# Kernel tuning notes

Measured on AMD Instinct MI355X. Metric: run time of the kernel, lower is better.

## Reference

```python
import jax, jax.numpy as jnp
import numpy as np

N = 100000
E = 1600000
DIN = 128
DH = 128
DOUT = 32
G = 64
EPS = 1e-5


def setup_inputs() -> dict:
    key = jax.random.key(0)
    ks = jax.random.split(key, 12)
    x = jax.random.normal(ks[0], (N, DIN), dtype=jnp.float32)
    edge_index = jax.random.randint(ks[1], (2, E), 0, N, dtype=jnp.int64)
    batch = jnp.sort(jax.random.randint(ks[2], (N,), 0, G, dtype=jnp.int64))
    # GCNConv weights (glorot-ish) + zero bias
    W1 = jax.random.normal(ks[3], (DIN, DH), dtype=jnp.float32) * (2.0 / (DIN + DH)) ** 0.5
    b1 = jnp.zeros((DH,), jnp.float32)
    W2 = jax.random.normal(ks[4], (DH, DH), dtype=jnp.float32) * (2.0 / (DH + DH)) ** 0.5
    b2 = jnp.zeros((DH,), jnp.float32)
    # BatchNorm affine params
    g1 = jnp.ones((DH,), jnp.float32); be1 = jnp.zeros((DH,), jnp.float32)
    g2 = jnp.ones((DH,), jnp.float32); be2 = jnp.zeros((DH,), jnp.float32)
    # Linear heads: kaiming normal fan_in relu, bias=0.001
    fw1 = jax.random.normal(ks[5], (DH, DH), dtype=jnp.float32) * (2.0 / DH) ** 0.5
    fb1 = jnp.full((DH,), 0.001, jnp.float32)
    fw2 = jax.random.normal(ks[6], (DH, DOUT), dtype=jnp.float32) * (2.0 / DH) ** 0.5
    fb2 = jnp.full((DOUT,), 0.001, jnp.float32)
    return dict(x=x, edge_index=edge_index, batch=batch, W1=W1, b1=b1, W2=W2, b2=b2,
                g1=g1, be1=be1, g2=g2, be2=be2, fw1=fw1, fb1=fb1, fw2=fw2, fb2=fb2)


def _gcn(x, src, dst, dinv, W, b):
    h = x @ W  # [N, F]
    norm = dinv[src] * dinv[dst]  # [E+N]
    agg = jax.ops.segment_sum(h[src] * norm[:, None], dst, num_segments=N)
    return agg + b


def _bn(h, gamma, beta):
    mu = h.mean(axis=0)
    var = h.var(axis=0)  # biased, matches torch BN training mode
    return (h - mu) * jax.lax.rsqrt(var + EPS) * gamma + beta


def reference(x, edge_index, batch, W1, b1, W2, b2, g1, be1, g2, be2, fw1, fb1, fw2, fb2):
    # add self-loops (PyG GCNConv default)
    loops = jnp.arange(N, dtype=edge_index.dtype)
    src = jnp.concatenate([edge_index[0], loops])
    dst = jnp.concatenate([edge_index[1], loops])
    deg = jax.ops.segment_sum(jnp.ones_like(dst, dtype=x.dtype), dst, num_segments=N)
    dinv = jnp.where(deg > 0, jax.lax.rsqrt(deg), 0.0)

    h = jax.nn.relu(_bn(_gcn(x, src, dst, dinv, W1, b1), g1, be1))
    h = jax.nn.relu(_bn(_gcn(h, src, dst, dinv, W2, b2), g2, be2))

    # global mean pool over graph ids
    sums = jax.ops.segment_sum(h, batch, num_segments=G)
    cnt = jax.ops.segment_sum(jnp.ones((N,), h.dtype), batch, num_segments=G)
    pooled = sums / jnp.maximum(cnt, 1.0)[:, None]  # [G, DH]

    z = jax.nn.relu(pooled @ fw1 + fb1)
    return jax.nn.softmax(z @ fw2 + fb2, axis=1)
```

## Files before the change

### kernel.cpp

```cpp
#include <hip/hip_runtime.h>
#include <hip/hip_bf16.h>
#include <stdint.h>

#define NN 100000
#define NE 1600000
#define DH 128
#define DOUT 32
#define NG 64
#define EPS 1e-5f

#define SCAN_BLK 1024
#define SCAN_NB ((NN + SCAN_BLK - 1) / SCAN_BLK)
#define NBUCKET 32
#define NRANGE 4
#define RANGE_SZ (NN / NRANGE)

typedef __attribute__((ext_vector_type(8))) unsigned short ushort8;
typedef __attribute__((ext_vector_type(8))) short bfv8;
typedef __attribute__((ext_vector_type(4))) float f32x4;
typedef __attribute__((ext_vector_type(4))) int intv4;
typedef __attribute__((ext_vector_type(2))) unsigned int uintv2;

__device__ __forceinline__ float b2f(unsigned short u) {
    return __uint_as_float(((unsigned int)u) << 16);
}
__device__ __forceinline__ unsigned int f2b(float f) {
    unsigned int u = __float_as_uint(f);
    return (u + 0x7fffu + ((u >> 16) & 1u)) >> 16;
}
__device__ __forceinline__ float blo(unsigned int v) { return __uint_as_float(v << 16); }
__device__ __forceinline__ float bhi(unsigned int v) { return __uint_as_float(v & 0xffff0000u); }


__global__ void k_count(const int* __restrict__ ei_dst, int* __restrict__ cnt) {
    int range = blockIdx.x & (NRANGE - 1);
    int lo = range * RANGE_SZ, hi = lo + RANGE_SZ;
    int i = (blockIdx.x >> 2) * blockDim.x + threadIdx.x;
    int stride = (gridDim.x >> 2) * blockDim.x;
    const intv4* d4 = reinterpret_cast<const intv4*>(ei_dst);
    for (int e = i; e < NE / 4; e += stride) {
        intv4 d = __builtin_nontemporal_load(d4 + e);
        if (d.x >= lo && d.x < hi) atomicAdd(&cnt[d.x], 1);
        if (d.y >= lo && d.y < hi) atomicAdd(&cnt[d.y], 1);
        if (d.z >= lo && d.z < hi) atomicAdd(&cnt[d.z], 1);
        if (d.w >= lo && d.w < hi) atomicAdd(&cnt[d.w], 1);
    }
}

__global__ void k_fill(const int* __restrict__ ei, int* __restrict__ cursor, int* __restrict__ csr) {
    int range = blockIdx.x & (NRANGE - 1);
    int lo = range * RANGE_SZ, hi = lo + RANGE_SZ;
    int i = (blockIdx.x >> 2) * blockDim.x + threadIdx.x;
    int stride = (gridDim.x >> 2) * blockDim.x;
    const intv4* s4 = reinterpret_cast<const intv4*>(ei);
    const intv4* d4 = reinterpret_cast<const intv4*>(ei + NE);
    for (int e = i; e < NE / 4; e += stride) {
        intv4 s = __builtin_nontemporal_load(s4 + e);
        intv4 d = __builtin_nontemporal_load(d4 + e);
        if (d.x >= lo && d.x < hi) csr[atomicAdd(&cursor[d.x], 1)] = s.x;
        if (d.y >= lo && d.y < hi) csr[atomicAdd(&cursor[d.y], 1)] = s.y;
        if (d.z >= lo && d.z < hi) csr[atomicAdd(&cursor[d.z], 1)] = s.z;
        if (d.w >= lo && d.w < hi) csr[atomicAdd(&cursor[d.w], 1)] = s.w;
    }
}

__global__ void k_gbound(const int* __restrict__ batch, int* __restrict__ first, int* __restrict__ last) {
    int i = blockIdx.x * blockDim.x + threadIdx.x;
    if (i >= NN) return;
    int g = batch[i];
    if (i == 0 || batch[i - 1] != g) first[g] = i;
    if (i == NN - 1 || batch[i + 1] != g) last[g] = i + 1;
}

__global__ void k_scan_partial(const int* __restrict__ cnt, int* __restrict__ bsum) {
    __shared__ int sdata[256];
    int blk = blockIdx.x, t = threadIdx.x;
    int base = blk * SCAN_BLK + t * 4;
    int s = 0;
#pragma unroll
    for (int q = 0; q < 4; q++) { int idx = base + q; if (idx < NN) s += cnt[idx]; }
    sdata[t] = s; __syncthreads();
    for (int o = 128; o; o >>= 1) { if (t < o) sdata[t] += sdata[t + o]; __syncthreads(); }
    if (t == 0) bsum[blk] = sdata[0];
}

__global__ void k_scan_top(const int* __restrict__ bsum, int* __restrict__ bscan, int* __restrict__ rowptr,
                           const int* __restrict__ first, const int* __restrict__ last, int* __restrict__ gcnt) {
    __shared__ int sd[128];
    int t = threadIdx.x;
    int v = (t < SCAN_NB) ? bsum[t] : 0;
    sd[t] = v; __syncthreads();
    for (int o = 1; o < 128; o <<= 1) {
        int add = (t >= o) ? sd[t - o] : 0;
        __syncthreads();
        sd[t] += add;
        __syncthreads();
    }
    if (t < SCAN_NB) bscan[t] = sd[t] - v;
    if (t == 127) rowptr[NN] = sd[127];
    if (t < NG) gcnt[t] = last[t] - first[t];
}

__global__ void k_scan_final(int* __restrict__ cnt, const int* __restrict__ bscan,
                             int* __restrict__ rowptr, float* __restrict__ dinv) {
    __shared__ int sdata[256];
    int blk = blockIdx.x, t = threadIdx.x;
    int base = blk * SCAN_BLK + t * 4;
    int v[4]; int s = 0;
#pragma unroll
    for (int q = 0; q < 4; q++) { int idx = base + q; v[q] = (idx < NN) ? cnt[idx] : 0; s += v[q]; }
    sdata[t] = s; __syncthreads();
    for (int o = 1; o < 256; o <<= 1) {
        int add = (t >= o) ? sdata[t - o] : 0;
        __syncthreads();
        sdata[t] += add;
        __syncthreads();
    }
    int offset = bscan[blk] + sdata[t] - s;
#pragma unroll
    for (int q = 0; q < 4; q++) {
        int idx = base + q;
        if (idx < NN) {
            rowptr[idx] = offset;
            cnt[idx] = offset;
            dinv[idx] = rsqrtf((float)(v[q] + 1));
            offset += v[q];
        }
    }
}


__global__ void k_prepw(const float* __restrict__ W1, const float* __restrict__ W2,
                        unsigned short* __restrict__ WT1, unsigned short* __restrict__ WT2) {
    int i = blockIdx.x * blockDim.x + threadIdx.x;
    int sel = i >> 14;
    int j = i & 16383;
    int k = j >> 7, n = j & 127;
    const float* W = sel ? W2 : W1;
    unsigned short* WT = sel ? WT2 : WT1;
    WT[n * 128 + k] = (unsigned short)f2b(W[j]);
}


template <bool BN, typename AT>
__global__ __launch_bounds__(256) void k_gemm(const AT* __restrict__ A, const unsigned short* __restrict__ WTg,
                                              unsigned short* __restrict__ C, const float* __restrict__ rowscale,
                                              const float* __restrict__ scale, const float* __restrict__ shift) {
    __shared__ unsigned char lds[65536];
    unsigned char* As = lds;
    unsigned char* Ws = lds + 32768;
    int row0 = blockIdx.x * 128;
    int t = threadIdx.x;
    int l = t & 63;
    int w = t >> 6;

    if constexpr (sizeof(AT) == 4) {
#pragma unroll
        for (int q = 0; q < 16; q++) {
            int idx = q * 256 + t;
            int r = idx >> 5, c4 = idx & 31;
            float4 v = make_float4(0.f, 0.f, 0.f, 0.f);
            if (row0 + r < NN) v = reinterpret_cast<const float4*>(A)[(size_t)(row0 + r) * 32 + c4];
            ushort4 u;
            u.x = (unsigned short)f2b(v.x);
            u.y = (unsigned short)f2b(v.y);
            u.z = (unsigned short)f2b(v.z);
            u.w = (unsigned short)f2b(v.w);
            int off = r * 256 + ((c4 * 8) ^ ((r & 7) << 4));
            *reinterpret_cast<ushort4*>(As + off) = u;
        }
    } else {
#pragma unroll
        for (int q = 0; q < 8; q++) {
            int idx = q * 256 + t;
            int r = idx >> 4, c8 = idx & 15;
// ... 38 lines not shown
            a[m] = *reinterpret_cast<const bfv8*>(As + r * 256 + (kb ^ ((r & 7) << 4)));
        }
        bfv8 b[8];
#pragma unroll
        for (int n = 0; n < 8; n++) {
            int r = n * 16 + lrow;
            b[n] = *reinterpret_cast<const bfv8*>(Ws + r * 256 + (kb ^ ((r & 7) << 4)));
        }
#pragma unroll
        for (int m = 0; m < 2; m++)
#pragma unroll
            for (int n = 0; n < 8; n++)
                acc[m][n] = __builtin_amdgcn_mfma_f32_16x16x32_bf16(a[m], b[n], acc[m][n], 0, 0, 0);
    }

#pragma unroll
    for (int m = 0; m < 2; m++) {
#pragma unroll
        for (int rr = 0; rr < 4; rr++) {
            int grow = row0 + w * 32 + m * 16 + (l >> 4) * 4 + rr;
            if (grow < NN) {
                float rs = rowscale[grow];
#pragma unroll
                for (int n = 0; n < 8; n++) {
                    int col = n * 16 + (l & 15);
                    C[(size_t)grow * DH + col] = (unsigned short)f2b(acc[m][n][rr] * rs);
                }
            }
        }
    }
}


__global__ __launch_bounds__(256) void k_aggregate(const unsigned short* __restrict__ h, const int* __restrict__ rowptr,
                                                   const int* __restrict__ csr, const float* __restrict__ dinv,
                                                   unsigned short* __restrict__ agg, float* __restrict__ stats) {
    int lane = threadIdx.x & 63;
    int wv = threadIdx.x >> 6;
    int half = lane >> 5;
    int sl = lane & 31;
    const uintv2* h64 = reinterpret_cast<const uintv2*>(h);
    uintv2* agg64 = reinterpret_cast<uintv2*>(agg);
    int wid = blockIdx.x * 4 + wv;
    int nw = gridDim.x * 4;
    long long tlo = ((long long)wid * NE) / nw;
    long long thi = (wid == nw - 1) ? (long long)NE + 1 : (((long long)(wid + 1) * NE) / nw);

    int lo = 0, hi = NN;
    while (lo < hi) {
        int mid = (lo + hi) >> 1;
        if (rowptr[mid] < (int)tlo) lo = mid + 1; else hi = mid;
    }

    float s0 = 0.f, s1 = 0.f, s2 = 0.f, s3 = 0.f;
    float q0 = 0.f, q1 = 0.f, q2 = 0.f, q3 = 0.f;
    for (int i = lo; i < NN; i++) {
        int row = rowptr[i];
        if (row >= (int)thi) break;
        int end = rowptr[i + 1];
        int len = end - row;
        float di = dinv[i];
        float a0 = 0.f, a1 = 0.f, a2 = 0.f, a3 = 0.f;
        if (half == 0) {
            uintv2 sv = h64[(size_t)i * 32 + sl];
            a0 = blo(sv.x); a1 = bhi(sv.x); a2 = blo(sv.y); a3 = bhi(sv.y);
        }
        int hc = (len + 1 - half) >> 1;
        int tt = 0;
        for (; tt + 8 <= hc; tt += 8) {
            int eA = row + (tt << 1) + half;
            int n0 = __builtin_nontemporal_load(&csr[eA]);
            int n1 = __builtin_nontemporal_load(&csr[eA + 2]);
            int n2 = __builtin_nontemporal_load(&csr[eA + 4]);
            int n3 = __builtin_nontemporal_load(&csr[eA + 6]);
            int n4 = __builtin_nontemporal_load(&csr[eA + 8]);
            int n5 = __builtin_nontemporal_load(&csr[eA + 10]);
            int n6 = __builtin_nontemporal_load(&csr[eA + 12]);
            int n7 = __builtin_nontemporal_load(&csr[eA + 14]);
            uintv2 v0 = h64[(size_t)n0 * 32 + sl];
            uintv2 v1 = h64[(size_t)n1 * 32 + sl];
            uintv2 v2 = h64[(size_t)n2 * 32 + sl];
            uintv2 v3 = h64[(size_t)n3 * 32 + sl];
            uintv2 v4 = h64[(size_t)n4 * 32 + sl];
            uintv2 v5 = h64[(size_t)n5 * 32 + sl];
            uintv2 v6 = h64[(size_t)n6 * 32 + sl];
            uintv2 v7 = h64[(size_t)n7 * 32 + sl];
            a0 += blo(v0.x); a1 += bhi(v0.x); a2 += blo(v0.y); a3 += bhi(v0.y);
            a0 += blo(v1.x); a1 += bhi(v1.x); a2 += blo(v1.y); a3 += bhi(v1.y);
            a0 += blo(v2.x); a1 += bhi(v2.x); a2 += blo(v2.y); a3 += bhi(v2.y);
            a0 += blo(v3.x); a1 += bhi(v3.x); a2 += blo(v3.y); a3 += bhi(v3.y);
            a0 += blo(v4.x); a1 += bhi(v4.x); a2 += blo(v4.y); a3 += bhi(v4.y);
            a0 += blo(v5.x); a1 += bhi(v5.x); a2 += blo(v5.y); a3 += bhi(v5.y);
            a0 += blo(v6.x); a1 += bhi(v6.x); a2 += blo(v6.y); a3 += bhi(v6.y);
            a0 += blo(v7.x); a1 += bhi(v7.x); a2 += blo(v7.y); a3 += bhi(v7.y);
        }
        for (; tt + 4 <= hc; tt += 4) {
            int eA = row + (tt << 1) + half;
            int n0 = __builtin_nontemporal_load(&csr[eA]);
            int n1 = __builtin_nontemporal_load(&csr[eA + 2]);
            int n2 = __builtin_nontemporal_load(&csr[eA + 4]);
            int n3 = __builtin_nontemporal_load(&csr[eA + 6]);
            uintv2 v0 = h64[(size_t)n0 * 32 + sl];
            uintv2 v1 = h64[(size_t)n1 * 32 + sl];
            uintv2 v2 = h64[(size_t)n2 * 32 + sl];
            uintv2 v3 = h64[(size_t)n3 * 32 + sl];
            a0 += blo(v0.x); a1 += bhi(v0.x); a2 += blo(v0.y); a3 += bhi(v0.y);
            a0 += blo(v1.x); a1 += bhi(v1.x); a2 += blo(v1.y); a3 += bhi(v1.y);
            a0 += blo(v2.x); a1 += bhi(v2.x); a2 += blo(v2.y); a3 += bhi(v2.y);
            a0 += blo(v3.x); a1 += bhi(v3.x); a2 += blo(v3.y); a3 += bhi(v3.y);
        }
        for (; tt < hc; tt++) {
            int e = row + (tt << 1) + half;
            int n = __builtin_nontemporal_load(&csr[e]);
            uintv2 v = h64[(size_t)n * 32 + sl];
            a0 += blo(v.x); a1 += bhi(v.x); a2 += blo(v.y); a3 += bhi(v.y);
        }
        a0 += __shfl_xor(a0, 32);
        a1 += __shfl_xor(a1, 32);
        a2 += __shfl_xor(a2, 32);
        a3 += __shfl_xor(a3, 32);
        a0 *= di; a1 *= di; a2 *= di; a3 *= di;
        if (half == 0) {
            uintv2 o;
            o.x = f2b(a0) | (f2b(a1) << 16);
            o.y = f2b(a2) | (f2b(a3) << 16);
            __builtin_nontemporal_store(o, agg64 + ((size_t)i * 32 + sl));
            s0 += a0; q0 += a0 * a0;
            s1 += a1; q1 += a1 * a1;
            s2 += a2; q2 += a2 * a2;
            s3 += a3; q3 += a3 * a3;
        }
    }
    if (half == 0) {
        float* b = stats + (size_t)(wid & (NBUCKET - 1)) * 256;
        atomicAdd(&b[sl * 4 + 0], s0);
        atomicAdd(&b[sl * 4 + 1], s1);
        atomicAdd(&b[sl * 4 + 2], s2);
        atomicAdd(&b[sl * 4 + 3], s3);
        atomicAdd(&b[128 + sl * 4 + 0], q0);
        atomicAdd(&b[128 + sl * 4 + 1], q1);
        atomicAdd(&b[128 + sl * 4 + 2], q2);
        atomicAdd(&b[128 + sl * 4 + 3], q3);
    }
}

__global__ void k_bnparams(const float* __restrict__ stats, const float* __restrict__ gamma,
                           const float* __restrict__ beta, float* __restrict__ scale, float* __restrict__ shift) {
    int j = threadIdx.x;
    float su = 0.f, sq = 0.f;
    for (int b = 0; b < NBUCKET; b++) { su += stats[b * 256 + j]; sq += stats[b * 256 + 128 + j]; }
    float mu = su * (1.f / NN);
    float var = sq * (1.f / NN) - mu * mu;
    float rs = rsqrtf(var + EPS);
    float sc = rs * gamma[j];
    scale[j] = sc;
    shift[j] = beta[j] - mu * sc;
}


#define POOL_CHUNK 64

__global__ __launch_bounds__(64) void k_pool(const unsigned short* __restrict__ agg, const int* __restrict__ batch,
                                             const float* __restrict__ scale, const float* __restrict__ shift,
                                             float* __restrict__ pooled) {
    int j = threadIdx.x;
    const unsigned int* a32 = reinterpret_cast<const unsigned int*>(agg);
    int n0 = blockIdx.x * POOL_CHUNK;
    int n1 = n0 + POOL_CHUNK; if (n1 > NN) n1 = NN;
    float sc0 = scale[j * 2], sh0 = shift[j * 2];
    float sc1 = scale[j * 2 + 1], sh1 = shift[j * 2 + 1];
    int gcur = batch[n0];
    float acc0 = 0.f, acc1 = 0.f;
    for (int i = n0; i < n1; i++) {
        int g = batch[i];
        if (g != gcur) {
            atomicAdd(&pooled[(size_t)gcur * DH + j * 2], acc0);
            atomicAdd(&pooled[(size_t)gcur * DH + j * 2 + 1], acc1);
            acc0 = acc1 = 0.f; gcur = g;
        }
        unsigned int v = a32[(size_t)i * 64 + j];
        acc0 += fmaxf(blo(v) * sc0 + sh0, 0.f);
        acc1 += fmaxf(bhi(v) * sc1 + sh1, 0.f);
    }
    atomicAdd(&pooled[(size_t)gcur * DH + j * 2], acc0);
    atomicAdd(&pooled[(size_t)gcur * DH + j * 2 + 1], acc1);
}


__global__ __launch_bounds__(128) void k_head(const float* __restrict__ pooled, const int* __restrict__ gcnt,
// ... 36 lines not shown
    const int*   batch = (const int*)d_in[2];
    const float* W1    = (const float*)d_in[3];
    const float* W2    = (const float*)d_in[5];
    const float* g1    = (const float*)d_in[7];
    const float* be1   = (const float*)d_in[8];
    const float* g2    = (const float*)d_in[9];
    const float* be2   = (const float*)d_in[10];
    const float* fw1   = (const float*)d_in[11];
    const float* fb1   = (const float*)d_in[12];
    const float* fw2   = (const float*)d_in[13];
    const float* fb2   = (const float*)d_in[14];
    float* out = (float*)d_out;

    char* w = (char*)d_ws;
    unsigned short* hbuf = (unsigned short*)w;  w += (size_t)NN * DH * 2;
    unsigned short* abuf = (unsigned short*)w;  w += (size_t)NN * DH * 2;
    int*   csr    = (int*)w;    w += (size_t)NE * 4;
    int*   rowptr = (int*)w;    w += (size_t)(NN + 1) * 4;  w = align256p(w);
    float* dinv   = (float*)w;  w += (size_t)NN * 4;
    int*   bsum   = (int*)w;    w += 512 * 4;
    int*   bscan  = (int*)w;    w += 512 * 4;
    float* scale1 = (float*)w;  w += DH * 4;
    float* shift1 = (float*)w;  w += DH * 4;
    float* scale2 = (float*)w;  w += DH * 4;
    float* shift2 = (float*)w;  w += DH * 4;
    unsigned short* WT1g = (unsigned short*)w;  w += (size_t)DH * DH * 2;
    unsigned short* WT2g = (unsigned short*)w;  w += (size_t)DH * DH * 2;
    w = align256p(w);
    char* zstart  = w;
    int*   cnt    = (int*)w;    w += (size_t)NN * 4;
    int*   gfirst = (int*)w;    w += 64 * 4;
    int*   glast  = (int*)w;    w += 64 * 4;
    int*   gcnt   = (int*)w;    w += 64 * 4;
    float* stats1 = (float*)w;  w += (size_t)NBUCKET * 256 * 4;
    float* stats2 = (float*)w;  w += (size_t)NBUCKET * 256 * 4;
    float* pooled = (float*)w;  w += (size_t)NG * DH * 4;
    size_t zbytes = (size_t)(w - zstart);
    size_t need = (size_t)(w - (char*)d_ws);
    if (ws_size < need) return;

    hipMemsetAsync(zstart, 0, zbytes, stream);

    k_prepw<<<128, 256, 0, stream>>>(W1, W2, WT1g, WT2g);
    k_count<<<1024, 256, 0, stream>>>(ei + NE, cnt);
    k_gbound<<<(NN + 255) / 256, 256, 0, stream>>>(batch, gfirst, glast);
    k_scan_partial<<<SCAN_NB, 256, 0, stream>>>(cnt, bsum);
    k_scan_top<<<1, 128, 0, stream>>>(bsum, bscan, rowptr, gfirst, glast, gcnt);
    k_scan_final<<<SCAN_NB, 256, 0, stream>>>(cnt, bscan, rowptr, dinv);
    k_fill<<<1024, 256, 0, stream>>>(ei, cnt, csr);

    int gemm_grid = (NN + 127) / 128;

    k_gemm<false, float><<<gemm_grid, 256, 0, stream>>>(x, WT1g, hbuf, dinv, nullptr, nullptr);
    k_aggregate<<<2048, 256, 0, stream>>>(hbuf, rowptr, csr, dinv, abuf, stats1);
    k_bnparams<<<1, 128, 0, stream>>>(stats1, g1, be1, scale1, shift1);

    k_gemm<true, unsigned short><<<gemm_grid, 256, 0, stream>>>(abuf, WT2g, hbuf, dinv, scale1, shift1);
    k_aggregate<<<2048, 256, 0, stream>>>(hbuf, rowptr, csr, dinv, abuf, stats2);
    k_bnparams<<<1, 128, 0, stream>>>(stats2, g2, be2, scale2, shift2);

    int pool_grid = (NN + POOL_CHUNK - 1) / POOL_CHUNK;
    k_pool<<<pool_grid, 64, 0, stream>>>(abuf, batch, scale2, shift2, pooled);
    k_head<<<NG, 128, 0, stream>>>(pooled, gcnt, fw1, fb1, fw2, fb2, out);
}
```

Before: 503.6 us.

## Fuse prep kernels, fold BN params into aggregate, process two rows per wave

Merges the degree count, graph-boundary and weight-transpose kernels into one launch, and computes the BN scale/shift in the last-finishing block of the aggregate kernel using a completion counter, which removes separate tiny launches. The aggregate loop now handles two destination rows at once with predicated 4-wide gathers, replacing the 8/4/1 unrolled tail loops. It also drops the nontemporal csr loads and agg stores and switches to 128-thread blocks. Predication wastes gather slots when the two rows differ in degree, and the last-block pattern relies on threadfence ordering.

```diff
diff --git a/kernel.cpp b/kernel.cpp
--- a/kernel.cpp
+++ b/kernel.cpp
@@ -15,6 +15,10 @@
 #define NRANGE 4
 #define RANGE_SZ (NN / NRANGE)
 
+#define PREP_COUNT_BLKS 1024
+#define PREP_GB_BLKS ((NN + 255) / 256)
+#define PREP_PW_BLKS 128
+
 typedef __attribute__((ext_vector_type(8))) unsigned short ushort8;
 typedef __attribute__((ext_vector_type(8))) short bfv8;
 typedef __attribute__((ext_vector_type(4))) float f32x4;
@@ -32,18 +36,98 @@
 __device__ __forceinline__ float bhi(unsigned int v) { return __uint_as_float(v & 0xffff0000u); }
 
 
-__global__ void k_count(const int* __restrict__ ei_dst, int* __restrict__ cnt) {
-    int range = blockIdx.x & (NRANGE - 1);
-    int lo = range * RANGE_SZ, hi = lo + RANGE_SZ;
-    int i = (blockIdx.x >> 2) * blockDim.x + threadIdx.x;
-    int stride = (gridDim.x >> 2) * blockDim.x;
-    const intv4* d4 = reinterpret_cast<const intv4*>(ei_dst);
-    for (int e = i; e < NE / 4; e += stride) {
-        intv4 d = __builtin_nontemporal_load(d4 + e);
-        if (d.x >= lo && d.x < hi) atomicAdd(&cnt[d.x], 1);
-        if (d.y >= lo && d.y < hi) atomicAdd(&cnt[d.y], 1);
-        if (d.z >= lo && d.z < hi) atomicAdd(&cnt[d.z], 1);
-        if (d.w >= lo && d.w < hi) atomicAdd(&cnt[d.w], 1);
+__global__ void k_prep(const int* __restrict__ ei_dst, int* __restrict__ cnt,
+                       const int* __restrict__ batch, int* __restrict__ gfirst, int* __restrict__ glast,
+                       const float* __restrict__ W1, const float* __restrict__ W2,
+                       unsigned short* __restrict__ WT1, unsigned short* __restrict__ WT2) {
+    int bid = blockIdx.x;
+    int t = threadIdx.x;
+    if (bid < PREP_COUNT_BLKS) {
+        int range = bid & (NRANGE - 1);
+        int lo = range * RANGE_SZ, hi = lo + RANGE_SZ;
+        int i = (bid >> 2) * 256 + t;
+        int stride = (PREP_COUNT_BLKS >> 2) * 256;
+        const intv4* d4 = reinterpret_cast<const intv4*>(ei_dst);
+        for (int e = i; e < NE / 4; e += stride) {
+            intv4 d = __builtin_nontemporal_load(d4 + e);
+            if (d.x >= lo && d.x < hi) atomicAdd(&cnt[d.x], 1);
+            if (d.y >= lo && d.y < hi) atomicAdd(&cnt[d.y], 1);
+            if (d.z >= lo && d.z < hi) atomicAdd(&cnt[d.z], 1);
+            if (d.w >= lo && d.w < hi) atomicAdd(&cnt[d.w], 1);
+        }
+    } else if (bid < PREP_COUNT_BLKS + PREP_GB_BLKS) {
+        int i = (bid - PREP_COUNT_BLKS) * 256 + t;
+        if (i < NN) {
+            int g = batch[i];
+            if (i == 0 || batch[i - 1] != g) gfirst[g] = i;
+            if (i == NN - 1 || batch[i + 1] != g) glast[g] = i + 1;
+        }
+    } else {
+        int i = (bid - PREP_COUNT_BLKS - PREP_GB_BLKS) * 256 + t;
+        int sel = i >> 14;
+        int j = i & 16383;
+        int k = j >> 7, n = j & 127;
+        const float* W = sel ? W2 : W1;
+        unsigned short* WT = sel ? WT2 : WT1;
+        WT[n * 128 + k] = (unsigned short)f2b(W[j]);
+    }
+}
+
+
+__global__ void k_scan_partial(const int* __restrict__ cnt, int* __restrict__ bsum) {
+    __shared__ int sdata[256];
+    int blk = blockIdx.x, t = threadIdx.x;
+    int base = blk * SCAN_BLK + t * 4;
+    int s = 0;
+#pragma unroll
+    for (int q = 0; q < 4; q++) { int idx = base + q; if (idx < NN) s += cnt[idx]; }
+    sdata[t] = s; __syncthreads();
+    for (int o = 128; o; o >>= 1) { if (t < o) sdata[t] += sdata[t + o]; __syncthreads(); }
+    if (t == 0) bsum[blk] = sdata[0];
+}
+
+__global__ void k_scan_top(const int* __restrict__ bsum, int* __restrict__ bscan, int* __restrict__ rowptr,
+                           const int* __restrict__ first, const int* __restrict__ last, int* __restrict__ gcnt) {
+    __shared__ int sd[128];
+    int t = threadIdx.x;
+    int v = (t < SCAN_NB) ? bsum[t] : 0;
+    sd[t] = v; __syncthreads();
+    for (int o = 1; o < 128; o <<= 1) {
+        int add = (t >= o) ? sd[t - o] : 0;
+        __syncthreads();
+        sd[t] += add;
+        __syncthreads();
+    }
+    if (t < SCAN_NB) bscan[t] = sd[t] - v;
+    if (t == 127) rowptr[NN] = sd[127];
+    if (t < NG) gcnt[t] = last[t] - first[t];
+}
+
+__global__ void k_scan_final(int* __restrict__ cnt, const int* __restrict__ bscan,
+                             int* __restrict__ rowptr, float* __restrict__ dinv) {
+    __shared__ int sdata[256];
+    int blk = blockIdx.x, t = threadIdx.x;
+    int base = blk * SCAN_BLK + t * 4;
+    int v[4]; int s = 0;
+#pragma unroll
+    for (int q = 0; q < 4; q++) { int idx = base + q; v[q] = (idx < NN) ? cnt[idx] : 0; s += v[q]; }
+    sdata[t] = s; __syncthreads();
+    for (int o = 1; o < 256; o <<= 1) {
+        int add = (t >= o) ? sdata[t - o] : 0;
+        __syncthreads();
+        sdata[t] += add;
+        __syncthreads();
+    }
+    int offset = bscan[blk] + sdata[t] - s;
+#pragma unroll
+    for (int q = 0; q < 4; q++) {
+        int idx = base + q;
+        if (idx < NN) {
+            rowptr[idx] = offset;
+            cnt[idx] = offset;
+            dinv[idx] = rsqrtf((float)(v[q] + 1));
+            offset += v[q];
+        }
     }
 }
 
@@ -64,83 +148,6 @@
     }
 }
 
-__global__ void k_gbound(const int* __restrict__ batch, int* __restrict__ first, int* __restrict__ last) {
-    int i = blockIdx.x * blockDim.x + threadIdx.x;
-    if (i >= NN) return;
-    int g = batch[i];
-    if (i == 0 || batch[i - 1] != g) first[g] = i;
-    if (i == NN - 1 || batch[i + 1] != g) last[g] = i + 1;
-}
-
-__global__ void k_scan_partial(const int* __restrict__ cnt, int* __restrict__ bsum) {
-    __shared__ int sdata[256];
-    int blk = blockIdx.x, t = threadIdx.x;
-    int base = blk * SCAN_BLK + t * 4;
-    int s = 0;
-#pragma unroll
-    for (int q = 0; q < 4; q++) { int idx = base + q; if (idx < NN) s += cnt[idx]; }
-    sdata[t] = s; __syncthreads();
-    for (int o = 128; o; o >>= 1) { if (t < o) sdata[t] += sdata[t + o]; __syncthreads(); }
-    if (t == 0) bsum[blk] = sdata[0];
-}
-
-__global__ void k_scan_top(const int* __restrict__ bsum, int* __restrict__ bscan, int* __restrict__ rowptr,
-                           const int* __restrict__ first, const int* __restrict__ last, int* __restrict__ gcnt) {
-    __shared__ int sd[128];
-    int t = threadIdx.x;
-    int v = (t < SCAN_NB) ? bsum[t] : 0;
-    sd[t] = v; __syncthreads();
-    for (int o = 1; o < 128; o <<= 1) {
-        int add = (t >= o) ? sd[t - o] : 0;
-        __syncthreads();
-        sd[t] += add;
-        __syncthreads();
-    }
-    if (t < SCAN_NB) bscan[t] = sd[t] - v;
-    if (t == 127) rowptr[NN] = sd[127];
-    if (t < NG) gcnt[t] = last[t] - first[t];
-}
-
-__global__ void k_scan_final(int* __restrict__ cnt, const int* __restrict__ bscan,
-                             int* __restrict__ rowptr, float* __restrict__ dinv) {
-    __shared__ int sdata[256];
-    int blk = blockIdx.x, t = threadIdx.x;
-    int base = blk * SCAN_BLK + t * 4;
-    int v[4]; int s = 0;
-#pragma unroll
-    for (int q = 0; q < 4; q++) { int idx = base + q; v[q] = (idx < NN) ? cnt[idx] : 0; s += v[q]; }
-    sdata[t] = s; __syncthreads();
-    for (int o = 1; o < 256; o <<= 1) {
-        int add = (t >= o) ? sdata[t - o] : 0;
-        __syncthreads();
-        sdata[t] += add;
-        __syncthreads();
-    }
-    int offset = bscan[blk] + sdata[t] - s;
-#pragma unroll
-    for (int q = 0; q < 4; q++) {
-        int idx = base + q;
-        if (idx < NN) {
-            rowptr[idx] = offset;
-            cnt[idx] = offset;
-            dinv[idx] = rsqrtf((float)(v[q] + 1));
-            offset += v[q];
-        }
-    }
-}
-
-
-__global__ void k_prepw(const float* __restrict__ W1, const float* __restrict__ W2,
-                        unsigned short* __restrict__ WT1, unsigned short* __restrict__ WT2) {
-    int i = blockIdx.x * blockDim.x + threadIdx.x;
-    int sel = i >> 14;
-    int j = i & 16383;
-    int k = j >> 7, n = j & 127;
-    const float* W = sel ? W2 : W1;
-    unsigned short* WT = sel ? WT2 : WT1;
-    WT[n * 128 + k] = (unsigned short)f2b(W[j]);
-}
-
 
 template <bool BN, typename AT>
 __global__ __launch_bounds__(256) void k_gemm(const AT* __restrict__ A, const unsigned short* __restrict__ WTg,
@@ -245,19 +252,23 @@
 }
 
 
-__global__ __launch_bounds__(256) void k_aggregate(const unsigned short* __restrict__ h, const int* __restrict__ rowptr,
+__global__ __launch_bounds__(128) void k_aggregate(const unsigned short* __restrict__ h, const int* __restrict__ rowptr,
                                                    const int* __restrict__ csr, const float* __restrict__ dinv,
-                                                   unsigned short* __restrict__ agg, float* __restrict__ stats) {
+                                                   unsigned short* __restrict__ agg, float* __restrict__ stats,
+                                                   const float* __restrict__ gamma, const float* __restrict__ beta,
+                                                   float* __restrict__ scale, float* __restrict__ shift,
+                                                   int* __restrict__ done) {
     int lane = threadIdx.x & 63;
     int wv = threadIdx.x >> 6;
     int half = lane >> 5;
     int sl = lane & 31;
     const uintv2* h64 = reinterpret_cast<const uintv2*>(h);
     uintv2* agg64 = reinterpret_cast<uintv2*>(agg);
-    int wid = blockIdx.x * 4 + wv;
-    int nw = gridDim.x * 4;
+    int wid = blockIdx.x * 2 + wv;
+    int nw = gridDim.x * 2;
     long long tlo = ((long long)wid * NE) / nw;
     long long thi = (wid == nw - 1) ? (long long)NE + 1 : (((long long)(wid + 1) * NE) / nw);
+    int thii = (int)thi;
 
     int lo = 0, hi = NN;
     while (lo < hi) {
@@ -267,82 +278,97 @@
 
     float s0 = 0.f, s1 = 0.f, s2 = 0.f, s3 = 0.f;
     float q0 = 0.f, q1 = 0.f, q2 = 0.f, q3 = 0.f;
-    for (int i = lo; i < NN; i++) {
-        int row = rowptr[i];
-        if (row >= (int)thi) break;
-        int end = rowptr[i + 1];
-        int len = end - row;
-        float di = dinv[i];
+    int i = lo;
+    int rowA = (i < NN) ? rowptr[i] : NE;
+    while (i < NN && rowA < thii) {
+        int endA = rowptr[i + 1];
+        int iB = i + 1;
+        int rowB = endA;
+        bool hasB = (iB < NN) && (rowB < thii);
+        int endB = hasB ? rowptr[iB + 1] : rowB;
+        int lenA = endA - rowA;
+        int lenB = endB - rowB;
+
+        float diA = dinv[i];
+        float diB = hasB ? dinv[iB] : 0.f;
         float a0 = 0.f, a1 = 0.f, a2 = 0.f, a3 = 0.f;
+        float b0 = 0.f, b1 = 0.f, b2 = 0.f, b3 = 0.f;
         if (half == 0) {
             uintv2 sv = h64[(size_t)i * 32 + sl];
             a0 = blo(sv.x); a1 = bhi(sv.x); a2 = blo(sv.y); a3 = bhi(sv.y);
-        }
-        int hc = (len + 1 - half) >> 1;
-        int tt = 0;
-        for (; tt + 8 <= hc; tt += 8) {
-            int eA = row + (tt << 1) + half;
-            int n0 = __builtin_nontemporal_load(&csr[eA]);
-            int n1 = __builtin_nontemporal_load(&csr[eA + 2]);
-            int n2 = __builtin_nontemporal_load(&csr[eA + 4]);
-            int n3 = __builtin_nontemporal_load(&csr[eA + 6]);
-            int n4 = __builtin_nontemporal_load(&csr[eA + 8]);
-            int n5 = __builtin_nontemporal_load(&csr[eA + 10]);
-            int n6 = __builtin_nontemporal_load(&csr[eA + 12]);
-            int n7 = __builtin_nontemporal_load(&csr[eA + 14]);
-            uintv2 v0 = h64[(size_t)n0 * 32 + sl];
-            uintv2 v1 = h64[(size_t)n1 * 32 + sl];
-            uintv2 v2 = h64[(size_t)n2 * 32 + sl];
-            uintv2 v3 = h64[(size_t)n3 * 32 + sl];
-            uintv2 v4 = h64[(size_t)n4 * 32 + sl];
-            uintv2 v5 = h64[(size_t)n5 * 32 + sl];
-            uintv2 v6 = h64[(size_t)n6 * 32 + sl];
-            uintv2 v7 = h64[(size_t)n7 * 32 + sl];
-            a0 += blo(v0.x); a1 += bhi(v0.x); a2 += blo(v0.y); a3 += bhi(v0.y);
-            a0 += blo(v1.x); a1 += bhi(v1.x); a2 += blo(v1.y); a3 += bhi(v1.y);
-            a0 += blo(v2.x); a1 += bhi(v2.x); a2 += blo(v2.y); a3 += bhi(v2.y);
-            a0 += blo(v3.x); a1 += bhi(v3.x); a2 += blo(v3.y); a3 += bhi(v3.y);
-            a0 += blo(v4.x); a1 += bhi(v4.x); a2 += blo(v4.y); a3 += bhi(v4.y);
-            a0 += blo(v5.x); a1 += bhi(v5.x); a2 += blo(v5.y); a3 += bhi(v5.y);
-            a0 += blo(v6.x); a1 += bhi(v6.x); a2 += blo(v6.y); a3 += bhi(v6.y);
-            a0 += blo(v7.x); a1 += bhi(v7.x); a2 += blo(v7.y); a3 += bhi(v7.y);
-        }
-        for (; tt + 4 <= hc; tt += 4) {
-            int eA = row + (tt << 1) + half;
-            int n0 = __builtin_nontemporal_load(&csr[eA]);
-            int n1 = __builtin_nontemporal_load(&csr[eA + 2]);
-            int n2 = __builtin_nontemporal_load(&csr[eA + 4]);
-            int n3 = __builtin_nontemporal_load(&csr[eA + 6]);
-            uintv2 v0 = h64[(size_t)n0 * 32 + sl];
-            uintv2 v1 = h64[(size_t)n1 * 32 + sl];
-            uintv2 v2 = h64[(size_t)n2 * 32 + sl];
-            uintv2 v3 = h64[(size_t)n3 * 32 + sl];
-            a0 += blo(v0.x); a1 += bhi(v0.x); a2 += blo(v0.y); a3 += bhi(v0.y);
-            a0 += blo(v1.x); a1 += bhi(v1.x); a2 += blo(v1.y); a3 += bhi(v1.y);
-            a0 += blo(v2.x); a1 += bhi(v2.x); a2 += blo(v2.y); a3 += bhi(v2.y);
-            a0 += blo(v3.x); a1 += bhi(v3.x); a2 += blo(v3.y); a3 += bhi(v3.y);
-        }
-        for (; tt < hc; tt++) {
-            int e = row + (tt << 1) + half;
-            int n = __builtin_nontemporal_load(&csr[e]);
-            uintv2 v = h64[(size_t)n * 32 + sl];
-            a0 += blo(v.x); a1 += bhi(v.x); a2 += blo(v.y); a3 += bhi(v.y);
-        }
-        a0 += __shfl_xor(a0, 32);
-        a1 += __shfl_xor(a1, 32);
-        a2 += __shfl_xor(a2, 32);
-        a3 += __shfl_xor(a3, 32);
-        a0 *= di; a1 *= di; a2 *= di; a3 *= di;
+            if (hasB) {
+                uintv2 tv = h64[(size_t)iB * 32 + sl];
+                b0 = blo(tv.x); b1 = bhi(tv.x); b2 = blo(tv.y); b3 = bhi(tv.y);
+            }
+        }
+        int hcA = (lenA + 1 - half) >> 1;
+        int hcB = hasB ? ((lenB + 1 - half) >> 1) : 0;
+        int hmU = ((lenA + 1) >> 1);
+        int hmB = ((lenB + 1) >> 1);
+        if (hasB && hmB > hmU) hmU = hmB;
+
+        for (int tt = 0; tt < hmU; tt += 4) {
+            int baseA = rowA + (tt << 1) + half;
+            int baseB = rowB + (tt << 1) + half;
+            bool pA0 = (tt + 0) < hcA, pA1 = (tt + 1) < hcA, pA2 = (tt + 2) < hcA, pA3 = (tt + 3) < hcA;
+            bool pB0 = (tt + 0) < hcB, pB1 = (tt + 1) < hcB, pB2 = (tt + 2) < hcB, pB3 = (tt + 3) < hcB;
+            int iA0 = pA0 ? csr[baseA + 0] : i;
+            int iA1 = pA1 ? csr[baseA + 2] : i;
+            int iA2 = pA2 ? csr[baseA + 4] : i;
+            int iA3 = pA3 ? csr[baseA + 6] : i;
+            int iB0 = pB0 ? csr[baseB + 0] : i;
+            int iB1 = pB1 ? csr[baseB + 2] : i;
+            int iB2 = pB2 ? csr[baseB + 4] : i;
+            int iB3 = pB3 ? csr[baseB + 6] : i;
+            uintv2 vA0 = h64[(size_t)iA0 * 32 + sl];
+            uintv2 vA1 = h64[(size_t)iA1 * 32 + sl];
+            uintv2 vA2 = h64[(size_t)iA2 * 32 + sl];
+            uintv2 vA3 = h64[(size_t)iA3 * 32 + sl];
+            uintv2 vB0 = h64[(size_t)iB0 * 32 + sl];
+            uintv2 vB1 = h64[(size_t)iB1 * 32 + sl];
+            uintv2 vB2 = h64[(size_t)iB2 * 32 + sl];
+            uintv2 vB3 = h64[(size_t)iB3 * 32 + sl];
+            a0 += pA0 ? blo(vA0.x) : 0.f; a1 += pA0 ? bhi(vA0.x) : 0.f;
+            a2 += pA0 ? blo(vA0.y) : 0.f; a3 += pA0 ? bhi(vA0.y) : 0.f;
+            a0 += pA1 ? blo(vA1.x) : 0.f; a1 += pA1 ? bhi(vA1.x) : 0.f;
+            a2 += pA1 ? blo(vA1.y) : 0.f; a3 += pA1 ? bhi(vA1.y) : 0.f;
+            a0 += pA2 ? blo(vA2.x) : 0.f; a1 += pA2 ? bhi(vA2.x) : 0.f;
+            a2 += pA2 ? blo(vA2.y) : 0.f; a3 += pA2 ? bhi(vA2.y) : 0.f;
+            a0 += pA3 ? blo(vA3.x) : 0.f; a1 += pA3 ? bhi(vA3.x) : 0.f;
+            a2 += pA3 ? blo(vA3.y) : 0.f; a3 += pA3 ? bhi(vA3.y) : 0.f;
+            b0 += pB0 ? blo(vB0.x) : 0.f; b1 += pB0 ? bhi(vB0.x) : 0.f;
+            b2 += pB0 ? blo(vB0.y) : 0.f; b3 += pB0 ? bhi(vB0.y) : 0.f;
+            b0 += pB1 ? blo(vB1.x) : 0.f; b1 += pB1 ? bhi(vB1.x) : 0.f;
+            b2 += pB1 ? blo(vB1.y) : 0.f; b3 += pB1 ? bhi(vB1.y) : 0.f;
+            b0 += pB2 ? blo(vB2.x) : 0.f; b1 += pB2 ? bhi(vB2.x) : 0.f;
+            b2 += pB2 ? blo(vB2.y) : 0.f; b3 += pB2 ? bhi(vB2.y) : 0.f;
+            b0 += pB3 ? blo(vB3.x) : 0.f; b1 += pB3 ? bhi(vB3.x) : 0.f;
+            b2 += pB3 ? blo(vB3.y) : 0.f; b3 += pB3 ? bhi(vB3.y) : 0.f;
+        }
+        a0 += __shfl_xor(a0, 32); a1 += __shfl_xor(a1, 32);
+        a2 += __shfl_xor(a2, 32); a3 += __shfl_xor(a3, 32);
+        b0 += __shfl_xor(b0, 32); b1 += __shfl_xor(b1, 32);
+        b2 += __shfl_xor(b2, 32); b3 += __shfl_xor(b3, 32);
+        a0 *= diA; a1 *= diA; a2 *= diA; a3 *= diA;
+        b0 *= diB; b1 *= diB; b2 *= diB; b3 *= diB;
         if (half == 0) {
             uintv2 o;
             o.x = f2b(a0) | (f2b(a1) << 16);
             o.y = f2b(a2) | (f2b(a3) << 16);
-            __builtin_nontemporal_store(o, agg64 + ((size_t)i * 32 + sl));
-            s0 += a0; q0 += a0 * a0;
-            s1 += a1; q1 += a1 * a1;
-            s2 += a2; q2 += a2 * a2;
-            s3 += a3; q3 += a3 * a3;
-        }
+            agg64[(size_t)i * 32 + sl] = o;
+            s0 += a0; q0 += a0 * a0; s1 += a1; q1 += a1 * a1;
+            s2 += a2; q2 += a2 * a2; s3 += a3; q3 += a3 * a3;
+            if (hasB) {
+                uintv2 p;
+                p.x = f2b(b0) | (f2b(b1) << 16);
+                p.y = f2b(b2) | (f2b(b3) << 16);
+                agg64[(size_t)iB * 32 + sl] = p;
+                s0 += b0; q0 += b0 * b0; s1 += b1; q1 += b1 * b1;
+                s2 += b2; q2 += b2 * b2; s3 += b3; q3 += b3 * b3;
+            }
+        }
+        i += hasB ? 2 : 1;
+        rowA = hasB ? endB : endA;
     }
     if (half == 0) {
         float* b = stats + (size_t)(wid & (NBUCKET - 1)) * 256;
@@ -355,19 +381,26 @@
         atomicAdd(&b[128 + sl * 4 + 2], q2);
         atomicAdd(&b[128 + sl * 4 + 3], q3);
     }
-}
-
-__global__ void k_bnparams(const float* __restrict__ stats, const float* __restrict__ gamma,
-                           const float* __restrict__ beta, float* __restrict__ scale, float* __restrict__ shift) {
-    int j = threadIdx.x;
-    float su = 0.f, sq = 0.f;
-    for (int b = 0; b < NBUCKET; b++) { su += stats[b * 256 + j]; sq += stats[b * 256 + 128 + j]; }
-    float mu = su * (1.f / NN);
-    float var = sq * (1.f / NN) - mu * mu;
-    float rs = rsqrtf(var + EPS);
-    float sc = rs * gamma[j];
-    scale[j] = sc;
-    shift[j] = beta[j] - mu * sc;
+
+    __shared__ int amlast;
+    __syncthreads();
+    if (threadIdx.x == 0) {
+        __threadfence();
+        amlast = (atomicAdd(done, 1) == (int)gridDim.x - 1) ? 1 : 0;
+    }
+    __syncthreads();
+    if (amlast) {
+        __threadfence();
+        int j = threadIdx.x;
+        float su = 0.f, sq = 0.f;
+        for (int bb = 0; bb < NBUCKET; bb++) { su += stats[bb * 256 + j]; sq += stats[bb * 256 + 128 + j]; }
+        float mu = su * (1.f / NN);
+        float var = sq * (1.f / NN) - mu * mu;
+        float rs = rsqrtf(var + EPS);
+        float sc = rs * gamma[j];
+        scale[j] = sc;
+        shift[j] = beta[j] - mu * sc;
+    }
 }
 
 
@@ -470,6 +503,8 @@
     int*   gfirst = (int*)w;    w += 64 * 4;
     int*   glast  = (int*)w;    w += 64 * 4;
     int*   gcnt   = (int*)w;    w += 64 * 4;
+    int*   done1  = (int*)w;    w += 64;
+    int*   done2  = (int*)w;    w += 64;
     float* stats1 = (float*)w;  w += (size_t)NBUCKET * 256 * 4;
     float* stats2 = (float*)w;  w += (size_t)NBUCKET * 256 * 4;
     float* pooled = (float*)w;  w += (size_t)NG * DH * 4;
@@ -479,9 +514,8 @@
 
     hipMemsetAsync(zstart, 0, zbytes, stream);
 
-    k_prepw<<<128, 256, 0, stream>>>(W1, W2, WT1g, WT2g);
-    k_count<<<1024, 256, 0, stream>>>(ei + NE, cnt);
-    k_gbound<<<(NN + 255) / 256, 256, 0, stream>>>(batch, gfirst, glast);
+    k_prep<<<PREP_COUNT_BLKS + PREP_GB_BLKS + PREP_PW_BLKS, 256, 0, stream>>>(
+        ei + NE, cnt, batch, gfirst, glast, W1, W2, WT1g, WT2g);
     k_scan_partial<<<SCAN_NB, 256, 0, stream>>>(cnt, bsum);
     k_scan_top<<<1, 128, 0, stream>>>(bsum, bscan, rowptr, gfirst, glast, gcnt);
     k_scan_final<<<SCAN_NB, 256, 0, stream>>>(cnt, bscan, rowptr, dinv);
@@ -490,12 +524,10 @@
     int gemm_grid = (NN + 127) / 128;
 
     k_gemm<false, float><<<gemm_grid, 256, 0, stream>>>(x, WT1g, hbuf, dinv, nullptr, nullptr);
-    k_aggregate<<<2048, 256, 0, stream>>>(hbuf, rowptr, csr, dinv, abuf, stats1);
-    k_bnparams<<<1, 128, 0, stream>>>(stats1, g1, be1, scale1, shift1);
+    k_aggregate<<<4096, 128, 0, stream>>>(hbuf, rowptr, csr, dinv, abuf, stats1, g1, be1, scale1, shift1, done1);
 
     k_gemm<true, unsigned short><<<gemm_grid, 256, 0, stream>>>(abuf, WT2g, hbuf, dinv, scale1, shift1);
-    k_aggregate<<<2048, 256, 0, stream>>>(hbuf, rowptr, csr, dinv, abuf, stats2);
-    k_bnparams<<<1, 128, 0, stream>>>(stats2, g2, be2, scale2, shift2);
+    k_aggregate<<<4096, 128, 0, stream>>>(hbuf, rowptr, csr, dinv, abuf, stats2, g2, be2, scale2, shift2, done2);
 
     int pool_grid = (NN + POOL_CHUNK - 1) / POOL_CHUNK;
     k_pool<<<pool_grid, 64, 0, stream>>>(abuf, batch, scale2, shift2, pooled);
```

After: 643.7 us. +27.8%, slower.

## Merge prep kernels and retune aggregate grid, block size and unrolling

Applied to the files above, without the earlier changes.

Count, group-boundary and weight-transpose kernels are merged into one launch with block-index dispatch, removing two kernel launches. The aggregate kernel goes from 2048 blocks of 256 threads to 12288 blocks of 128 threads, giving many more, shorter edge ranges. Its 8-way unrolled gather loop is dropped and nontemporal loads and stores become plain ones. More waves raise the count of atomic stats flushes and of partially processed boundary rows, and less unrolling means fewer loads in flight per wave.

```diff
diff --git a/kernel.cpp b/kernel.cpp
--- a/kernel.cpp
+++ b/kernel.cpp
@@ -15,6 +15,10 @@
 #define NRANGE 4
 #define RANGE_SZ (NN / NRANGE)
 
+#define PREP_COUNT_BLKS 1024
+#define PREP_GB_BLKS ((NN + 255) / 256)
+#define PREP_PW_BLKS 128
+
 typedef __attribute__((ext_vector_type(8))) unsigned short ushort8;
 typedef __attribute__((ext_vector_type(8))) short bfv8;
 typedef __attribute__((ext_vector_type(4))) float f32x4;
@@ -32,18 +36,98 @@
 __device__ __forceinline__ float bhi(unsigned int v) { return __uint_as_float(v & 0xffff0000u); }
 
 
-__global__ void k_count(const int* __restrict__ ei_dst, int* __restrict__ cnt) {
-    int range = blockIdx.x & (NRANGE - 1);
-    int lo = range * RANGE_SZ, hi = lo + RANGE_SZ;
-    int i = (blockIdx.x >> 2) * blockDim.x + threadIdx.x;
-    int stride = (gridDim.x >> 2) * blockDim.x;
-    const intv4* d4 = reinterpret_cast<const intv4*>(ei_dst);
-    for (int e = i; e < NE / 4; e += stride) {
-        intv4 d = __builtin_nontemporal_load(d4 + e);
-        if (d.x >= lo && d.x < hi) atomicAdd(&cnt[d.x], 1);
-        if (d.y >= lo && d.y < hi) atomicAdd(&cnt[d.y], 1);
-        if (d.z >= lo && d.z < hi) atomicAdd(&cnt[d.z], 1);
-        if (d.w >= lo && d.w < hi) atomicAdd(&cnt[d.w], 1);
+__global__ void k_prep(const int* __restrict__ ei_dst, int* __restrict__ cnt,
+                       const int* __restrict__ batch, int* __restrict__ gfirst, int* __restrict__ glast,
+                       const float* __restrict__ W1, const float* __restrict__ W2,
+                       unsigned short* __restrict__ WT1, unsigned short* __restrict__ WT2) {
+    int bid = blockIdx.x;
+    int t = threadIdx.x;
+    if (bid < PREP_COUNT_BLKS) {
+        int range = bid & (NRANGE - 1);
+        int lo = range * RANGE_SZ, hi = lo + RANGE_SZ;
+        int i = (bid >> 2) * 256 + t;
+        int stride = (PREP_COUNT_BLKS >> 2) * 256;
+        const intv4* d4 = reinterpret_cast<const intv4*>(ei_dst);
+        for (int e = i; e < NE / 4; e += stride) {
+            intv4 d = __builtin_nontemporal_load(d4 + e);
+            if (d.x >= lo && d.x < hi) atomicAdd(&cnt[d.x], 1);
+            if (d.y >= lo && d.y < hi) atomicAdd(&cnt[d.y], 1);
+            if (d.z >= lo && d.z < hi) atomicAdd(&cnt[d.z], 1);
+            if (d.w >= lo && d.w < hi) atomicAdd(&cnt[d.w], 1);
+        }
+    } else if (bid < PREP_COUNT_BLKS + PREP_GB_BLKS) {
+        int i = (bid - PREP_COUNT_BLKS) * 256 + t;
+        if (i < NN) {
+            int g = batch[i];
+            if (i == 0 || batch[i - 1] != g) gfirst[g] = i;
+            if (i == NN - 1 || batch[i + 1] != g) glast[g] = i + 1;
+        }
+    } else {
+        int i = (bid - PREP_COUNT_BLKS - PREP_GB_BLKS) * 256 + t;
+        int sel = i >> 14;
+        int j = i & 16383;
+        int k = j >> 7, n = j & 127;
+        const float* W = sel ? W2 : W1;
+        unsigned short* WT = sel ? WT2 : WT1;
+        WT[n * 128 + k] = (unsigned short)f2b(W[j]);
+    }
+}
+
+
+__global__ void k_scan_partial(const int* __restrict__ cnt, int* __restrict__ bsum) {
+    __shared__ int sdata[256];
+    int blk = blockIdx.x, t = threadIdx.x;
+    int base = blk * SCAN_BLK + t * 4;
+    int s = 0;
+#pragma unroll
+    for (int q = 0; q < 4; q++) { int idx = base + q; if (idx < NN) s += cnt[idx]; }
+    sdata[t] = s; __syncthreads();
+    for (int o = 128; o; o >>= 1) { if (t < o) sdata[t] += sdata[t + o]; __syncthreads(); }
+    if (t == 0) bsum[blk] = sdata[0];
+}
+
+__global__ void k_scan_top(const int* __restrict__ bsum, int* __restrict__ bscan, int* __restrict__ rowptr,
+                           const int* __restrict__ first, const int* __restrict__ last, int* __restrict__ gcnt) {
+    __shared__ int sd[128];
+    int t = threadIdx.x;
+    int v = (t < SCAN_NB) ? bsum[t] : 0;
+    sd[t] = v; __syncthreads();
+    for (int o = 1; o < 128; o <<= 1) {
+        int add = (t >= o) ? sd[t - o] : 0;
+        __syncthreads();
+        sd[t] += add;
+        __syncthreads();
+    }
+    if (t < SCAN_NB) bscan[t] = sd[t] - v;
+    if (t == 127) rowptr[NN] = sd[127];
+    if (t < NG) gcnt[t] = last[t] - first[t];
+}
+
+__global__ void k_scan_final(int* __restrict__ cnt, const int* __restrict__ bscan,
+                             int* __restrict__ rowptr, float* __restrict__ dinv) {
+    __shared__ int sdata[256];
+    int blk = blockIdx.x, t = threadIdx.x;
+    int base = blk * SCAN_BLK + t * 4;
+    int v[4]; int s = 0;
+#pragma unroll
+    for (int q = 0; q < 4; q++) { int idx = base + q; v[q] = (idx < NN) ? cnt[idx] : 0; s += v[q]; }
+    sdata[t] = s; __syncthreads();
+    for (int o = 1; o < 256; o <<= 1) {
+        int add = (t >= o) ? sdata[t - o] : 0;
+        __syncthreads();
+        sdata[t] += add;
+        __syncthreads();
+    }
+    int offset = bscan[blk] + sdata[t] - s;
+#pragma unroll
+    for (int q = 0; q < 4; q++) {
+        int idx = base + q;
+        if (idx < NN) {
+            rowptr[idx] = offset;
+            cnt[idx] = offset;
+            dinv[idx] = rsqrtf((float)(v[q] + 1));
+            offset += v[q];
+        }
     }
 }
 
@@ -64,83 +148,6 @@
     }
 }
 
-__global__ void k_gbound(const int* __restrict__ batch, int* __restrict__ first, int* __restrict__ last) {
-    int i = blockIdx.x * blockDim.x + threadIdx.x;
-    if (i >= NN) return;
-    int g = batch[i];
-    if (i == 0 || batch[i - 1] != g) first[g] = i;
-    if (i == NN - 1 || batch[i + 1] != g) last[g] = i + 1;
-}
-
-__global__ void k_scan_partial(const int* __restrict__ cnt, int* __restrict__ bsum) {
-    __shared__ int sdata[256];
-    int blk = blockIdx.x, t = threadIdx.x;
-    int base = blk * SCAN_BLK + t * 4;
-    int s = 0;
-#pragma unroll
-    for (int q = 0; q < 4; q++) { int idx = base + q; if (idx < NN) s += cnt[idx]; }
-    sdata[t] = s; __syncthreads();
-    for (int o = 128; o; o >>= 1) { if (t < o) sdata[t] += sdata[t + o]; __syncthreads(); }
-    if (t == 0) bsum[blk] = sdata[0];
-}
-
-__global__ void k_scan_top(const int* __restrict__ bsum, int* __restrict__ bscan, int* __restrict__ rowptr,
-                           const int* __restrict__ first, const int* __restrict__ last, int* __restrict__ gcnt) {
-    __shared__ int sd[128];
-    int t = threadIdx.x;
-    int v = (t < SCAN_NB) ? bsum[t] : 0;
-    sd[t] = v; __syncthreads();
-    for (int o = 1; o < 128; o <<= 1) {
-        int add = (t >= o) ? sd[t - o] : 0;
-        __syncthreads();
-        sd[t] += add;
-        __syncthreads();
-    }
-    if (t < SCAN_NB) bscan[t] = sd[t] - v;
-    if (t == 127) rowptr[NN] = sd[127];
-    if (t < NG) gcnt[t] = last[t] - first[t];
-}
-
-__global__ void k_scan_final(int* __restrict__ cnt, const int* __restrict__ bscan,
-                             int* __restrict__ rowptr, float* __restrict__ dinv) {
-    __shared__ int sdata[256];
-    int blk = blockIdx.x, t = threadIdx.x;
-    int base = blk * SCAN_BLK + t * 4;
-    int v[4]; int s = 0;
-#pragma unroll
-    for (int q = 0; q < 4; q++) { int idx = base + q; v[q] = (idx < NN) ? cnt[idx] : 0; s += v[q]; }
-    sdata[t] = s; __syncthreads();
-    for (int o = 1; o < 256; o <<= 1) {
-        int add = (t >= o) ? sdata[t - o] : 0;
-        __syncthreads();
-        sdata[t] += add;
-        __syncthreads();
-    }
-    int offset = bscan[blk] + sdata[t] - s;
-#pragma unroll
-    for (int q = 0; q < 4; q++) {
-        int idx = base + q;
-        if (idx < NN) {
-            rowptr[idx] = offset;
-            cnt[idx] = offset;
-            dinv[idx] = rsqrtf((float)(v[q] + 1));
-            offset += v[q];
-        }
-    }
-}
-
-
-__global__ void k_prepw(const float* __restrict__ W1, const float* __restrict__ W2,
-                        unsigned short* __restrict__ WT1, unsigned short* __restrict__ WT2) {
-    int i = blockIdx.x * blockDim.x + threadIdx.x;
-    int sel = i >> 14;
-    int j = i & 16383;
-    int k = j >> 7, n = j & 127;
-    const float* W = sel ? W2 : W1;
-    unsigned short* WT = sel ? WT2 : WT1;
-    WT[n * 128 + k] = (unsigned short)f2b(W[j]);
-}
-
 
 template <bool BN, typename AT>
 __global__ __launch_bounds__(256) void k_gemm(const AT* __restrict__ A, const unsigned short* __restrict__ WTg,
@@ -245,7 +252,7 @@
 }
 
 
-__global__ __launch_bounds__(256) void k_aggregate(const unsigned short* __restrict__ h, const int* __restrict__ rowptr,
+__global__ __launch_bounds__(128) void k_aggregate(const unsigned short* __restrict__ h, const int* __restrict__ rowptr,
                                                    const int* __restrict__ csr, const float* __restrict__ dinv,
                                                    unsigned short* __restrict__ agg, float* __restrict__ stats) {
     int lane = threadIdx.x & 63;
@@ -254,8 +261,8 @@
     int sl = lane & 31;
     const uintv2* h64 = reinterpret_cast<const uintv2*>(h);
     uintv2* agg64 = reinterpret_cast<uintv2*>(agg);
-    int wid = blockIdx.x * 4 + wv;
-    int nw = gridDim.x * 4;
+    int wid = blockIdx.x * 2 + wv;
+    int nw = gridDim.x * 2;
     long long tlo = ((long long)wid * NE) / nw;
     long long thi = (wid == nw - 1) ? (long long)NE + 1 : (((long long)(wid + 1) * NE) / nw);
 
@@ -280,39 +287,9 @@
         }
         int hc = (len + 1 - half) >> 1;
         int tt = 0;
-        for (; tt + 8 <= hc; tt += 8) {
-            int eA = row + (tt << 1) + half;
-            int n0 = __builtin_nontemporal_load(&csr[eA]);
-            int n1 = __builtin_nontemporal_load(&csr[eA + 2]);
-            int n2 = __builtin_nontemporal_load(&csr[eA + 4]);
-            int n3 = __builtin_nontemporal_load(&csr[eA + 6]);
-            int n4 = __builtin_nontemporal_load(&csr[eA + 8]);
-            int n5 = __builtin_nontemporal_load(&csr[eA + 10]);
-            int n6 = __builtin_nontemporal_load(&csr[eA + 12]);
-            int n7 = __builtin_nontemporal_load(&csr[eA + 14]);
-            uintv2 v0 = h64[(size_t)n0 * 32 + sl];
-            uintv2 v1 = h64[(size_t)n1 * 32 + sl];
-            uintv2 v2 = h64[(size_t)n2 * 32 + sl];
-            uintv2 v3 = h64[(size_t)n3 * 32 + sl];
-            uintv2 v4 = h64[(size_t)n4 * 32 + sl];
-            uintv2 v5 = h64[(size_t)n5 * 32 + sl];
-            uintv2 v6 = h64[(size_t)n6 * 32 + sl];
-            uintv2 v7 = h64[(size_t)n7 * 32 + sl];
-            a0 += blo(v0.x); a1 += bhi(v0.x); a2 += blo(v0.y); a3 += bhi(v0.y);
-            a0 += blo(v1.x); a1 += bhi(v1.x); a2 += blo(v1.y); a3 += bhi(v1.y);
-            a0 += blo(v2.x); a1 += bhi(v2.x); a2 += blo(v2.y); a3 += bhi(v2.y);
-            a0 += blo(v3.x); a1 += bhi(v3.x); a2 += blo(v3.y); a3 += bhi(v3.y);
-            a0 += blo(v4.x); a1 += bhi(v4.x); a2 += blo(v4.y); a3 += bhi(v4.y);
-            a0 += blo(v5.x); a1 += bhi(v5.x); a2 += blo(v5.y); a3 += bhi(v5.y);
-            a0 += blo(v6.x); a1 += bhi(v6.x); a2 += blo(v6.y); a3 += bhi(v6.y);
-            a0 += blo(v7.x); a1 += bhi(v7.x); a2 += blo(v7.y); a3 += bhi(v7.y);
-        }
         for (; tt + 4 <= hc; tt += 4) {
             int eA = row + (tt << 1) + half;
-            int n0 = __builtin_nontemporal_load(&csr[eA]);
-            int n1 = __builtin_nontemporal_load(&csr[eA + 2]);
-            int n2 = __builtin_nontemporal_load(&csr[eA + 4]);
-            int n3 = __builtin_nontemporal_load(&csr[eA + 6]);
+            int n0 = csr[eA], n1 = csr[eA + 2], n2 = csr[eA + 4], n3 = csr[eA + 6];
             uintv2 v0 = h64[(size_t)n0 * 32 + sl];
             uintv2 v1 = h64[(size_t)n1 * 32 + sl];
             uintv2 v2 = h64[(size_t)n2 * 32 + sl];
@@ -324,7 +301,7 @@
         }
         for (; tt < hc; tt++) {
             int e = row + (tt << 1) + half;
-            int n = __builtin_nontemporal_load(&csr[e]);
+            int n = csr[e];
             uintv2 v = h64[(size_t)n * 32 + sl];
             a0 += blo(v.x); a1 += bhi(v.x); a2 += blo(v.y); a3 += bhi(v.y);
         }
@@ -337,7 +314,7 @@
             uintv2 o;
             o.x = f2b(a0) | (f2b(a1) << 16);
             o.y = f2b(a2) | (f2b(a3) << 16);
-            __builtin_nontemporal_store(o, agg64 + ((size_t)i * 32 + sl));
+            agg64[(size_t)i * 32 + sl] = o;
             s0 += a0; q0 += a0 * a0;
             s1 += a1; q1 += a1 * a1;
             s2 += a2; q2 += a2 * a2;
@@ -479,9 +456,8 @@
 
     hipMemsetAsync(zstart, 0, zbytes, stream);
 
-    k_prepw<<<128, 256, 0, stream>>>(W1, W2, WT1g, WT2g);
-    k_count<<<1024, 256, 0, stream>>>(ei + NE, cnt);
-    k_gbound<<<(NN + 255) / 256, 256, 0, stream>>>(batch, gfirst, glast);
+    k_prep<<<PREP_COUNT_BLKS + PREP_GB_BLKS + PREP_PW_BLKS, 256, 0, stream>>>(
+        ei + NE, cnt, batch, gfirst, glast, W1, W2, WT1g, WT2g);
     k_scan_partial<<<SCAN_NB, 256, 0, stream>>>(cnt, bsum);
     k_scan_top<<<1, 128, 0, stream>>>(bsum, bscan, rowptr, gfirst, glast, gcnt);
     k_scan_final<<<SCAN_NB, 256, 0, stream>>>(cnt, bscan, rowptr, dinv);
@@ -490,11 +466,11 @@
     int gemm_grid = (NN + 127) / 128;
 
     k_gemm<false, float><<<gemm_grid, 256, 0, stream>>>(x, WT1g, hbuf, dinv, nullptr, nullptr);
-    k_aggregate<<<2048, 256, 0, stream>>>(hbuf, rowptr, csr, dinv, abuf, stats1);
+    k_aggregate<<<12288, 128, 0, stream>>>(hbuf, rowptr, csr, dinv, abuf, stats1);
     k_bnparams<<<1, 128, 0, stream>>>(stats1, g1, be1, scale1, shift1);
 
     k_gemm<true, unsigned short><<<gemm_grid, 256, 0, stream>>>(abuf, WT2g, hbuf, dinv, scale1, shift1);
-    k_aggregate<<<2048, 256, 0, stream>>>(hbuf, rowptr, csr, dinv, abuf, stats2);
+    k_aggregate<<<12288, 128, 0, stream>>>(hbuf, rowptr, csr, dinv, abuf, stats2);
     k_bnparams<<<1, 128, 0, stream>>>(stats2, g2, be2, scale2, shift2);
 
     int pool_grid = (NN + POOL_CHUNK - 1) / POOL_CHUNK;
```

After: 536.6 us. 6.6% more time.
